# Optimization experiments

Measured on AMD Instinct MI355X. Metric: run time of the kernel, lower is better.

## Reference

```python
import jax, jax.numpy as jnp
import numpy as np

N = 50000   # nodes (single node type)
E = 200000  # edges per relation
R = 2       # relations (etypes)
D = 256     # in_dim == out_dim
H = 8       # heads
DK = D // H # 32
SQRT_DK = float(np.sqrt(DK))


def setup_inputs() -> dict:
    key = jax.random.key(0)
    ks = jax.random.split(key, 12)
    wsc = 1.0 / np.sqrt(D)   # linear-layer scale
    rsc = 1.0 / np.sqrt(DK)  # xavier-ish scale for relation tensors
    return {
        "x": jax.random.normal(ks[0], (N, D), jnp.float32),
        "src": jax.random.randint(ks[1], (R, E), 0, N, jnp.int32),
        "dst": jax.random.randint(ks[2], (R, E), 0, N, jnp.int32),
        "Wk": jax.random.normal(ks[3], (D, D), jnp.float32) * wsc,
        "bk": jnp.zeros((D,), jnp.float32),
        "Wq": jax.random.normal(ks[4], (D, D), jnp.float32) * wsc,
        "bq": jnp.zeros((D,), jnp.float32),
        "Wv": jax.random.normal(ks[5], (D, D), jnp.float32) * wsc,
        "bv": jnp.zeros((D,), jnp.float32),
        "Wa": jax.random.normal(ks[6], (D, D), jnp.float32) * wsc,
        "ba": jnp.zeros((D,), jnp.float32),
        "rel_pri": jnp.ones((R, H), jnp.float32),
        "rel_att": jax.random.normal(ks[7], (R, H, DK, DK), jnp.float32) * rsc,
        "rel_msg": jax.random.normal(ks[8], (R, H, DK, DK), jnp.float32) * rsc,
        "skip": jnp.ones((1,), jnp.float32),
    }


def reference(x, src, dst, Wk, bk, Wq, bq, Wv, bv, Wa, ba, rel_pri, rel_att, rel_msg, skip):
    # Per-type K/Q/V projections (single node type) -> [N,H,DK]
    k = (x @ Wk + bk).reshape(N, H, DK)
    q = (x @ Wq + bq).reshape(N, H, DK)
    v = (x @ Wv + bv).reshape(N, H, DK)

    # edge_attention: per-relation bmm transform of gathered src features
    key_t = jnp.einsum('rehd,rhdf->rehf', k[src], rel_att)   # [R,E,H,DK]
    val = jnp.einsum('rehd,rhdf->rehf', v[src], rel_msg)     # [R,E,H,DK]
    att = (q[dst] * key_t).sum(-1) * rel_pri[:, None, :] / SQRT_DK  # [R,E,H]

    # segment softmax over incoming edges per (relation, dst node)
    seg = (dst + N * jnp.arange(R, dtype=dst.dtype)[:, None]).reshape(-1)  # [R*E]
    att_f = att.reshape(R * E, H)
    m = jax.ops.segment_max(att_f, seg, num_segments=R * N)
    m = jnp.where(jnp.isfinite(m), m, 0.0)  # empty segments -> never gathered
    e = jnp.exp(att_f - m[seg])
    den = jax.ops.segment_sum(e, seg, num_segments=R * N)
    attn = e / den[seg]                                       # [R*E,H]

    # weighted-sum scatter aggregation, then cross_reducer='mean' over relations
    h = jax.ops.segment_sum(attn[:, :, None] * val.reshape(R * E, H, DK), seg,
                            num_segments=R * N)               # [R*N,H,DK]
    t = h.reshape(R, N, D).mean(axis=0)                        # [N,D]

    # skip-gated output projection (dropout inactive in eval, use_norm=False)
    alpha = jax.nn.sigmoid(skip[0])
    return (t @ Wa + ba) * alpha + x * (1.0 - alpha)
```

## Files before the change

kernel.cpp:

```cpp
#include <hip/hip_runtime.h>
#include <hip/hip_bf16.h>
#include <math.h>

#define NN 50000
#define EE 200000
#define DD 256
#define HH 8
#define DKK 32
#define NSEG (2 * NN)
#define SCAN_BLOCKS ((NSEG + 1023) / 1024)
#define MPAD 50048
#define LDQKV 1280

constexpr float RSQRT_DK = 0.17677669529663687f;

__device__ __forceinline__ float bf_lo(unsigned u) { return __uint_as_float(u << 16); }
__device__ __forceinline__ float bf_hi(unsigned u) { return __uint_as_float(u & 0xffff0000u); }
__device__ __forceinline__ unsigned short f2bf(float f) {
    unsigned u = __float_as_uint(f);
    return (unsigned short)((u + 0x7fffu + ((u >> 16) & 1u)) >> 16);
}

typedef __attribute__((ext_vector_type(8))) short bf16x8;
typedef __attribute__((ext_vector_type(4))) float f32x4;

#define GLDS16(g, l)                                                                   \
    __builtin_amdgcn_global_load_lds((const __attribute__((address_space(1))) unsigned int*)(g), \
                                     (__attribute__((address_space(3))) unsigned int*)(l), 16, 0, 0)

__global__ void cast_x_kernel(const float* __restrict__ x, unsigned short* __restrict__ xb) {
    const size_t i = ((size_t)blockIdx.x * 256 + threadIdx.x) * 4;
    float4 v = *(const float4*)&x[i];
    ushort4 o;
    o.x = f2bf(v.x); o.y = f2bf(v.y); o.z = f2bf(v.z); o.w = f2bf(v.w);
    *(ushort4*)&xb[i] = o;
}

__global__ void fold_qkv_kernel(const float* __restrict__ Wq, const float* __restrict__ Wk,
                                const float* __restrict__ Wv, const float* __restrict__ bq,
                                const float* __restrict__ bk, const float* __restrict__ bv,
                                const float* __restrict__ rel_att, const float* __restrict__ rel_msg,
                                unsigned short* __restrict__ Wt, float* __restrict__ bb) {
    const int n = blockIdx.x, kk = threadIdx.x;
    if (n < 256) {
        Wt[(size_t)n * 256 + kk] = f2bf(Wq[(size_t)kk * 256 + n]);
        if (kk == 0) bb[n] = bq[n];
        return;
    }
    const int sec = (n - 256) >> 8;
    const int c = (n - 256) & 255;
    const int h = c >> 5, f = c & 31;
    const float* W    = (sec < 2) ? Wk : Wv;
    const float* bsrc = (sec < 2) ? bk : bv;
    const float* T = ((sec < 2) ? rel_att : rel_msg)
                   + (size_t)(sec & 1) * HH * DKK * DKK + (size_t)h * DKK * DKK + f;
    const float* wrow = &W[(size_t)kk * 256 + h * 32];
    float s = 0.f;
    #pragma unroll
    for (int d = 0; d < 32; ++d) s += wrow[d] * T[(size_t)d * 32];
    Wt[(size_t)n * 256 + kk] = f2bf(s);
    if (kk == 0) {
        float sb = 0.f;
        for (int d = 0; d < 32; ++d) sb += bsrc[h * 32 + d] * T[(size_t)d * 32];
        bb[n] = sb;
    }
}

__global__ void cast_wa_kernel(const float* __restrict__ Wa, unsigned short* __restrict__ Bt) {
    const int n = blockIdx.x, kk = threadIdx.x;
    Bt[(size_t)n * 256 + kk] = f2bf(Wa[(size_t)kk * 256 + n]);
}

__global__ __launch_bounds__(256) void mfma_gemm(
        const unsigned short* __restrict__ A, const unsigned short* __restrict__ Bt,
        const float* __restrict__ bias,
        unsigned short* __restrict__ Cbf, float* __restrict__ Cf,
        int M, int ldc, const float* __restrict__ xres, const float* __restrict__ skip) {
    __shared__ __align__(16) unsigned short As[3][8][64][8];
    __shared__ __align__(16) unsigned short Bs[3][8][64][8];
    const int t = threadIdx.x;
    const int w = t >> 6, l = t & 63;

    const int nwg = gridDim.x * gridDim.y;
    int lin = blockIdx.y * gridDim.x + blockIdx.x;
    {
        const int xcd = lin & 7, pos = lin >> 3;
        const int q = nwg >> 3, r = nwg & 7;
        lin = (xcd < r ? xcd * (q + 1) : r * (q + 1) + (xcd - r) * q) + pos;
    }
    const int n0 = (lin % gridDim.x) * 128;
    const int m0 = (lin / gridDim.x) * 128;
    const int wm = w & 1, wn = w >> 1;

    const int sr = l & 15, sq = l >> 4;
    const unsigned short* ga0 = A  + (size_t)(m0 + w * 16 + sr) * 256 + sq * 8;
    const unsigned short* ga1 = A  + (size_t)(m0 + (w + 4) * 16 + sr) * 256 + sq * 8;
    const unsigned short* gb0 = Bt + (size_t)(n0 + w * 16 + sr) * 256 + sq * 8;
    const unsigned short* gb1 = Bt + (size_t)(n0 + (w + 4) * 16 + sr) * 256 + sq * 8;

#define STAGE(buf, k0) do {                    \
        GLDS16(ga0 + (k0), &As[buf][w][0][0]); \
        GLDS16(ga1 + (k0), &As[buf][w + 4][0][0]); \
        GLDS16(gb0 + (k0), &Bs[buf][w][0][0]); \
        GLDS16(gb1 + (k0), &Bs[buf][w + 4][0][0]); } while (0)

    f32x4 acc[4][4];
    #pragma unroll
    for (int mi = 0; mi < 4; ++mi)
        #pragma unroll
        for (int ni = 0; ni < 4; ++ni) acc[mi][ni] = (f32x4){0.f, 0.f, 0.f, 0.f};

    STAGE(0, 0);
    STAGE(1, 32);
    #pragma unroll
    for (int it = 0; it < 8; ++it) {
        if (it < 7) { asm volatile("s_waitcnt vmcnt(4)" ::: "memory"); }
        else        { asm volatile("s_waitcnt vmcnt(0)" ::: "memory"); }
        __builtin_amdgcn_s_barrier();
        __builtin_amdgcn_sched_barrier(0);
        if (it < 6) {
            STAGE((it + 2) % 3, (it + 2) * 32);
        }
        const int b = it % 3;
        bf16x8 af[4], bfr[4];
        #pragma unroll
        for (int i = 0; i < 4; ++i) {
            af[i]  = *(const bf16x8*)&As[b][wm * 4 + i][l][0];
            bfr[i] = *(const bf16x8*)&Bs[b][wn * 4 + i][l][0];
        }
        #pragma unroll
        for (int mi = 0; mi < 4; ++mi)
            #pragma unroll
            for (int ni = 0; ni < 4; ++ni)
                acc[mi][ni] = __builtin_amdgcn_mfma_f32_16x16x32_bf16(af[mi], bfr[ni],
                                                                      acc[mi][ni], 0, 0, 0);
    }
    __syncthreads();

    unsigned short* ep = (w < 2) ? &As[0][0][0][0] : &Bs[0][0][0][0];
    ep += (w & 1) * 4096;
    const int q4 = l >> 4, c15 = l & 15;

    if (Cf == nullptr) {
        #pragma unroll
        for (int ni = 0; ni < 4; ++ni) {
            const float bcol = bias[n0 + wn * 64 + ni * 16 + c15];
            const int g = ni * 2 + (c15 >> 3);
            #pragma unroll
            for (int mi = 0; mi < 4; ++mi)
                #pragma unroll
                for (int p = 0; p < 4; ++p) {
                    const int row = mi * 16 + q4 * 4 + p;
                    ep[row * 64 + ((g ^ (row & 7)) << 3) + (c15 & 7)] =
                        f2bf(acc[mi][ni][p] + bcol);
                }
        }
        __syncthreads();
        const int rs = l >> 3, cc = l & 7;
        #pragma unroll
        for (int i = 0; i < 8; ++i) {
            const int rl = i * 8 + rs;
            const int row = m0 + wm * 64 + rl;
            if (row < M) {
                uint4 v = *(const uint4*)&ep[rl * 64 + ((cc ^ (rl & 7)) << 3)];
                *(uint4*)&Cbf[(size_t)row * (size_t)ldc + n0 + wn * 64 + cc * 8] = v;
            }
        }
    } else {
        const float alpha = 1.f / (1.f + __expf(-skip[0]));
        const float beta = 1.f - alpha;
        float* epf = (float*)ep;
        #pragma unroll
        for (int half = 0; half < 2; ++half) {
            __syncthreads();
            #pragma unroll
            for (int mi2 = 0; mi2 < 2; ++mi2) {
                const int mi = half * 2 + mi2;
                #pragma unroll
                for (int ni = 0; ni < 4; ++ni) {
                    const float bcol = bias[n0 + wn * 64 + ni * 16 + c15];
                    const int g = ni * 4 + (c15 >> 2);
                    #pragma unroll
                    for (int p = 0; p < 4; ++p) {
                        const int row = mi2 * 16 + q4 * 4 + p;
                        epf[row * 64 + ((g ^ (row & 7)) << 2) + (c15 & 3)] =
                            acc[mi][ni][p] + bcol;
                    }
                }
            }
            __syncthreads();
            const int cc = l & 15, rs = l >> 4;
            #pragma unroll
            for (int i = 0; i < 8; ++i) {
                const int rl = i * 4 + rs;
                const int row = m0 + wm * 64 + half * 32 + rl;
                if (row < M) {
                    const int col = n0 + wn * 64 + cc * 4;
                    float4 v = *(const float4*)&epf[rl * 64 + ((cc ^ (rl & 7)) << 2)];
                    float4 xr = *(const float4*)&xres[(size_t)row * 256 + col];
                    v.x = v.x * alpha + xr.x * beta;
                    v.y = v.y * alpha + xr.y * beta;
                    v.z = v.z * alpha + xr.z * beta;
                    v.w = v.w * alpha + xr.w * beta;
                    *(float4*)&Cf[(size_t)row * 256 + col] = v;
                }
            }
        }
    }
#undef STAGE
}

__global__ void count_kernel(const int* __restrict__ dst, int* __restrict__ cnt) {
    int e = blockIdx.x * 256 + threadIdx.x;
    if (e < 2 * EE) atomicAdd(&cnt[(e / EE) * NN + dst[e]], 1);
}

__global__ __launch_bounds__(1024) void scan_local_kernel(const int* __restrict__ cnt,
                                                          int* __restrict__ rowptr,
                                                          int* __restrict__ bsum) {
    __shared__ int sh[1024];
    const int t = threadIdx.x;
    const int idx = blockIdx.x * 1024 + t;
    const int c = (idx < NSEG) ? cnt[idx] : 0;
    sh[t] = c;
    __syncthreads();
    #pragma unroll
    for (int ofs = 1; ofs < 1024; ofs <<= 1) {
        int v = (t >= ofs) ? sh[t - ofs] : 0;
        __syncthreads();
        sh[t] += v;
        __syncthreads();
    }
    if (idx < NSEG) rowptr[idx] = sh[t] - c;
    if (t == 1023) bsum[blockIdx.x] = sh[1023];
}

__global__ void scan_bsum_kernel(int* __restrict__ bsum, int* __restrict__ rowptr) {
    __shared__ int sh[128];
    const int t = threadIdx.x;
    const int v = (t < SCAN_BLOCKS) ? bsum[t] : 0;
    sh[t] = v;
    __syncthreads();
    #pragma unroll
    for (int ofs = 1; ofs < 128; ofs <<= 1) {
        int u = (t >= ofs) ? sh[t - ofs] : 0;
        __syncthreads();
        sh[t] += u;
        __syncthreads();
    }
    if (t < SCAN_BLOCKS) bsum[t] = sh[t] - v;
    if (t == 127) rowptr[NSEG] = sh[127];
}

__global__ __launch_bounds__(1024) void scan_add_kernel(int* __restrict__ rowptr,
                                                        const int* __restrict__ bsum,
                                                        int* __restrict__ cursor) {
    const int idx = blockIdx.x * 1024 + threadIdx.x;
    if (idx < NSEG) {
        const int v = rowptr[idx] + bsum[blockIdx.x];
        rowptr[idx] = v;
        cursor[idx] = v;
    }
}

__global__ void scatter_kernel(const int* __restrict__ src, const int* __restrict__ dst,
                               int* __restrict__ cursor, int* __restrict__ csr_src) {
    int e = blockIdx.x * 256 + threadIdx.x;
    if (e >= 2 * EE) return;
    int seg = (e / EE) * NN + dst[e];
    int pos = atomicAdd(&cursor[seg], 1);
    csr_src[pos] = src[e];
}

__global__ void node_agg_kernel(const unsigned short* __restrict__ qkv,
                                const int* __restrict__ csr_src,
                                const int* __restrict__ rowptr,
                                const float* __restrict__ pri,
                                unsigned short* __restrict__ tt_bf) {
    const int wave = threadIdx.x >> 6, lane = threadIdx.x & 63;
    const int n = blockIdx.x * 4 + wave;
    const int h = lane >> 3;
    const int off = lane * 4;

    const uint2 qv = *(const uint2*)&qkv[(size_t)n * LDQKV + off];
    const float q0 = bf_lo(qv.x), q1 = bf_hi(qv.x), q2 = bf_lo(qv.y), q3 = bf_hi(qv.y);

    float4 tot = make_float4(0.f, 0.f, 0.f, 0.f);
    #pragma unroll
    for (int r = 0; r < 2; ++r) {
        const float prm = pri[r * HH + h] * RSQRT_DK;
        const int seg = r * NN + n;
        const int j0 = rowptr[seg], j1 = rowptr[seg + 1];
        const size_t kbase = 256 + (size_t)r * 256 + off;
        const size_t vbase = 768 + (size_t)r * 256 + off;
        float4 acc = make_float4(0.f, 0.f, 0.f, 0.f);
        float den = 0.f;
        for (int j = j0; j < j1; ++j) {
            const int s = csr_src[j];
            const size_t rowb = (size_t)s * LDQKV;
            const uint2 kv = *(const uint2*)&qkv[rowb + kbase];
            const uint2 vv = *(const uint2*)&qkv[rowb + vbase];
            float p = q0 * bf_lo(kv.x) + q1 * bf_hi(kv.x)
                    + q2 * bf_lo(kv.y) + q3 * bf_hi(kv.y);
            p += __shfl_xor(p, 1);
            p += __shfl_xor(p, 2);
            p += __shfl_xor(p, 4);
            const float a = __expf(p * prm);
            den += a;
            acc.x += a * bf_lo(vv.x);
            acc.y += a * bf_hi(vv.x);
            acc.z += a * bf_lo(vv.y);
            acc.w += a * bf_hi(vv.y);
        }
        const float wgt = (den > 0.f) ? 0.5f / den : 0.f;
        tot.x += acc.x * wgt; tot.y += acc.y * wgt;
        tot.z += acc.z * wgt; tot.w += acc.w * wgt;
    }
    ushort4 ob;
    ob.x = f2bf(tot.x); ob.y = f2bf(tot.y); ob.z = f2bf(tot.z); ob.w = f2bf(tot.w);
    *(ushort4*)&tt_bf[(size_t)n * 256 + off] = ob;
}

extern "C" void kernel_launch(void* const* d_in, const int* in_sizes, int n_in,
                              void* d_out, int out_size, void* d_ws, size_t ws_size,
                              hipStream_t stream) {
    const float* x       = (const float*)d_in[0];
    const int*   src     = (const int*)d_in[1];
    const int*   dst     = (const int*)d_in[2];
    const float* Wk      = (const float*)d_in[3];
    const float* bk      = (const float*)d_in[4];
    const float* Wq      = (const float*)d_in[5];
    const float* bq      = (const float*)d_in[6];
    const float* Wv      = (const float*)d_in[7];
    const float* bv      = (const float*)d_in[8];
    const float* Wa      = (const float*)d_in[9];
    const float* ba      = (const float*)d_in[10];
    const float* rel_pri = (const float*)d_in[11];
    const float* rel_att = (const float*)d_in[12];
    const float* rel_msg = (const float*)d_in[13];
    const float* skip    = (const float*)d_in[14];
    float* out = (float*)d_out;
    char* ws = (char*)d_ws;

    const size_t ND = (size_t)NN * DD;
    size_t off = 0;
    unsigned short* x_bf   = (unsigned short*)(ws + off); off += (size_t)MPAD * DD * 2;
    unsigned short* qkv_bf = (unsigned short*)(ws + off); off += (size_t)NN * LDQKV * 2;
    unsigned short* tt_bf  = (unsigned short*)(ws + off); off += (size_t)MPAD * DD * 2;
    unsigned short* wqkv_t = (unsigned short*)(ws + off); off += (size_t)LDQKV * 256 * 2;
    unsigned short* wa_t   = (unsigned short*)(ws + off); off += (size_t)256 * 256 * 2;
    float*          bb     = (float*)(ws + off);          off += LDQKV * 4;
    int*            cnt    = (int*)(ws + off);            off += (size_t)NSEG * 4;
    int*            rowptr = (int*)(ws + off);            off += (size_t)(NSEG + 1) * 4;
    int*            cursor = (int*)(ws + off);            off += (size_t)NSEG * 4;
    int*            bsum   = (int*)(ws + off);            off += 128 * 4;
    int*            csr_src= (int*)(ws + off);            off += (size_t)2 * EE * 4;
    if (ws_size < off) return;

    cast_x_kernel<<<(int)(ND / 1024), 256, 0, stream>>>(x, x_bf);
    fold_qkv_kernel<<<LDQKV, 256, 0, stream>>>(Wq, Wk, Wv, bq, bk, bv,
                                               rel_att, rel_msg, wqkv_t, bb);
    cast_wa_kernel<<<256, 256, 0, stream>>>(Wa, wa_t);

    dim3 g_qkv(LDQKV / 128, MPAD / 128);
    mfma_gemm<<<g_qkv, 256, 0, stream>>>(x_bf, wqkv_t, bb, qkv_bf, nullptr,
                                         NN, LDQKV, nullptr, nullptr);

    hipMemsetAsync(cnt, 0, (size_t)NSEG * 4, stream);
    const int eg = (2 * EE + 255) / 256;
    count_kernel<<<eg, 256, 0, stream>>>(dst, cnt);
    scan_local_kernel<<<SCAN_BLOCKS, 1024, 0, stream>>>(cnt, rowptr, bsum);
    scan_bsum_kernel<<<1, 128, 0, stream>>>(bsum, rowptr);
    scan_add_kernel<<<SCAN_BLOCKS, 1024, 0, stream>>>(rowptr, bsum, cursor);
    scatter_kernel<<<eg, 256, 0, stream>>>(src, dst, cursor, csr_src);

    node_agg_kernel<<<NN / 4, 256, 0, stream>>>(qkv_bf, csr_src, rowptr,
                                                rel_pri, tt_bf);

    dim3 g_out(DD / 128, MPAD / 128);
    mfma_gemm<<<g_out, 256, 0, stream>>>(tt_bf, wa_t, ba, nullptr, out,
                                         NN, DD, x, skip);
}
```

Measured before the change: 377.2 us.

## Split node aggregation across relations and edge halves with prefetch; fuse Wa cast

The node aggregation kernel now gives each relation its own wave, and each wave splits into two half-waves that take alternating edges. Each lane loads 16 bytes of K and V and prefetches the next edge's rows. The two relation partial sums are combined through shared memory after a block barrier. The separate Wa transpose-cast kernel is folded into the fold_qkv launch as extra blocks, removing one launch. This is meant to raise memory-level parallelism and occupancy on the irregular gathers, at the cost of an LDS round-trip, a sync, and half the lanes sitting idle during the final write.

```diff
diff --git a/kernel.cpp b/kernel.cpp
--- a/kernel.cpp
+++ b/kernel.cpp
@@ -40,8 +40,14 @@
                                 const float* __restrict__ Wv, const float* __restrict__ bq,
                                 const float* __restrict__ bk, const float* __restrict__ bv,
                                 const float* __restrict__ rel_att, const float* __restrict__ rel_msg,
+                                const float* __restrict__ Wa, unsigned short* __restrict__ wa_t,
                                 unsigned short* __restrict__ Wt, float* __restrict__ bb) {
     const int n = blockIdx.x, kk = threadIdx.x;
+    if (n >= 1280) {
+        const int nn = n - 1280;
+        wa_t[(size_t)nn * 256 + kk] = f2bf(Wa[(size_t)kk * 256 + nn]);
+        return;
+    }
     if (n < 256) {
         Wt[(size_t)n * 256 + kk] = f2bf(Wq[(size_t)kk * 256 + n]);
         if (kk == 0) bb[n] = bq[n];
@@ -64,11 +70,6 @@
         for (int d = 0; d < 32; ++d) sb += bsrc[h * 32 + d] * T[(size_t)d * 32];
         bb[n] = sb;
     }
-}
-
-__global__ void cast_wa_kernel(const float* __restrict__ Wa, unsigned short* __restrict__ Bt) {
-    const int n = blockIdx.x, kk = threadIdx.x;
-    Bt[(size_t)n * 256 + kk] = f2bf(Wa[(size_t)kk * 256 + n]);
 }
 
 __global__ __launch_bounds__(256) void mfma_gemm(
@@ -272,53 +273,93 @@
     csr_src[pos] = src[e];
 }
 
-__global__ void node_agg_kernel(const unsigned short* __restrict__ qkv,
-                                const int* __restrict__ csr_src,
-                                const int* __restrict__ rowptr,
-                                const float* __restrict__ pri,
-                                unsigned short* __restrict__ tt_bf) {
-    const int wave = threadIdx.x >> 6, lane = threadIdx.x & 63;
-    const int n = blockIdx.x * 4 + wave;
-    const int h = lane >> 3;
-    const int off = lane * 4;
-
-    const uint2 qv = *(const uint2*)&qkv[(size_t)n * LDQKV + off];
+__global__ __launch_bounds__(512) void node_agg_kernel(
+        const unsigned short* __restrict__ qkv,
+        const int* __restrict__ csr_src,
+        const int* __restrict__ rowptr,
+        const float* __restrict__ pri,
+        unsigned short* __restrict__ tt_bf) {
+    __shared__ float sh[4][256];
+    const int w = threadIdx.x >> 6, lane = threadIdx.x & 63;
+    const int nl = w >> 1, r = w & 1;
+    const int n = blockIdx.x * 4 + nl;
+    const int lh = lane & 31;
+    const int eh = lane >> 5;
+    const int h = lh >> 2;
+    const size_t coff = (size_t)lh * 8;
+
+    const uint4 qv = *(const uint4*)&qkv[(size_t)n * LDQKV + coff];
     const float q0 = bf_lo(qv.x), q1 = bf_hi(qv.x), q2 = bf_lo(qv.y), q3 = bf_hi(qv.y);
-
-    float4 tot = make_float4(0.f, 0.f, 0.f, 0.f);
-    #pragma unroll
-    for (int r = 0; r < 2; ++r) {
-        const float prm = pri[r * HH + h] * RSQRT_DK;
-        const int seg = r * NN + n;
-        const int j0 = rowptr[seg], j1 = rowptr[seg + 1];
-        const size_t kbase = 256 + (size_t)r * 256 + off;
-        const size_t vbase = 768 + (size_t)r * 256 + off;
-        float4 acc = make_float4(0.f, 0.f, 0.f, 0.f);
-        float den = 0.f;
-        for (int j = j0; j < j1; ++j) {
-            const int s = csr_src[j];
-            const size_t rowb = (size_t)s * LDQKV;
-            const uint2 kv = *(const uint2*)&qkv[rowb + kbase];
-            const uint2 vv = *(const uint2*)&qkv[rowb + vbase];
-            float p = q0 * bf_lo(kv.x) + q1 * bf_hi(kv.x)
-                    + q2 * bf_lo(kv.y) + q3 * bf_hi(kv.y);
-            p += __shfl_xor(p, 1);
-            p += __shfl_xor(p, 2);
-            p += __shfl_xor(p, 4);
-            const float a = __expf(p * prm);
-            den += a;
-            acc.x += a * bf_lo(vv.x);
-            acc.y += a * bf_hi(vv.x);
-            acc.z += a * bf_lo(vv.y);
-            acc.w += a * bf_hi(vv.y);
-        }
-        const float wgt = (den > 0.f) ? 0.5f / den : 0.f;
-        tot.x += acc.x * wgt; tot.y += acc.y * wgt;
-        tot.z += acc.z * wgt; tot.w += acc.w * wgt;
-    }
-    ushort4 ob;
-    ob.x = f2bf(tot.x); ob.y = f2bf(tot.y); ob.z = f2bf(tot.z); ob.w = f2bf(tot.w);
-    *(ushort4*)&tt_bf[(size_t)n * 256 + off] = ob;
+    const float q4_ = bf_lo(qv.z), q5 = bf_hi(qv.z), q6 = bf_lo(qv.w), q7 = bf_hi(qv.w);
+
+    const float prm = pri[r * HH + h] * RSQRT_DK;
+    const int seg = r * NN + n;
+    const int j0 = rowptr[seg], j1 = rowptr[seg + 1];
+    const size_t kbase = 256 + (size_t)r * 256 + coff;
+    const size_t vbase = 768 + (size_t)r * 256 + coff;
+
+    float a0 = 0.f, a1 = 0.f, a2 = 0.f, a3 = 0.f, a4 = 0.f, a5 = 0.f, a6 = 0.f, a7 = 0.f;
+    float den = 0.f;
+
+    int j = j0 + eh;
+    uint4 kv, vv;
+    bool valid = j < j1;
+    if (valid) {
+        const size_t rowb = (size_t)csr_src[j] * LDQKV;
+        kv = *(const uint4*)&qkv[rowb + kbase];
+        vv = *(const uint4*)&qkv[rowb + vbase];
+    }
+    while (valid) {
+        const int jn = j + 2;
+        const bool validn = jn < j1;
+        uint4 kvn, vvn;
+        if (validn) {
+            const size_t rowb = (size_t)csr_src[jn] * LDQKV;
+            kvn = *(const uint4*)&qkv[rowb + kbase];
+            vvn = *(const uint4*)&qkv[rowb + vbase];
+        }
+        float p = q0 * bf_lo(kv.x) + q1 * bf_hi(kv.x) + q2 * bf_lo(kv.y) + q3 * bf_hi(kv.y)
+                + q4_ * bf_lo(kv.z) + q5 * bf_hi(kv.z) + q6 * bf_lo(kv.w) + q7 * bf_hi(kv.w);
+        p += __shfl_xor(p, 1);
+        p += __shfl_xor(p, 2);
+        const float a = __expf(p * prm);
+        den += a;
+        a0 += a * bf_lo(vv.x); a1 += a * bf_hi(vv.x);
+        a2 += a * bf_lo(vv.y); a3 += a * bf_hi(vv.y);
+        a4 += a * bf_lo(vv.z); a5 += a * bf_hi(vv.z);
+        a6 += a * bf_lo(vv.w); a7 += a * bf_hi(vv.w);
+        kv = kvn; vv = vvn; j = jn; valid = validn;
+    }
+    den += __shfl_xor(den, 32);
+    a0 += __shfl_xor(a0, 32); a1 += __shfl_xor(a1, 32);
+    a2 += __shfl_xor(a2, 32); a3 += __shfl_xor(a3, 32);
+    a4 += __shfl_xor(a4, 32); a5 += __shfl_xor(a5, 32);
+    a6 += __shfl_xor(a6, 32); a7 += __shfl_xor(a7, 32);
+    const float wgt = (den > 0.f) ? 0.5f / den : 0.f;
+
+    if (r == 0 && eh == 0) {
+        sh[nl][0 * 32 + lh] = a0 * wgt; sh[nl][1 * 32 + lh] = a1 * wgt;
+        sh[nl][2 * 32 + lh] = a2 * wgt; sh[nl][3 * 32 + lh] = a3 * wgt;
+        sh[nl][4 * 32 + lh] = a4 * wgt; sh[nl][5 * 32 + lh] = a5 * wgt;
+        sh[nl][6 * 32 + lh] = a6 * wgt; sh[nl][7 * 32 + lh] = a7 * wgt;
+    }
+    __syncthreads();
+    if (r == 1 && eh == 0) {
+        const float t0 = sh[nl][0 * 32 + lh] + a0 * wgt;
+        const float t1 = sh[nl][1 * 32 + lh] + a1 * wgt;
+        const float t2 = sh[nl][2 * 32 + lh] + a2 * wgt;
+        const float t3 = sh[nl][3 * 32 + lh] + a3 * wgt;
+        const float t4 = sh[nl][4 * 32 + lh] + a4 * wgt;
+        const float t5 = sh[nl][5 * 32 + lh] + a5 * wgt;
+        const float t6 = sh[nl][6 * 32 + lh] + a6 * wgt;
+        const float t7 = sh[nl][7 * 32 + lh] + a7 * wgt;
+        uint4 o;
+        o.x = (unsigned)f2bf(t0) | ((unsigned)f2bf(t1) << 16);
+        o.y = (unsigned)f2bf(t2) | ((unsigned)f2bf(t3) << 16);
+        o.z = (unsigned)f2bf(t4) | ((unsigned)f2bf(t5) << 16);
+        o.w = (unsigned)f2bf(t6) | ((unsigned)f2bf(t7) << 16);
+        *(uint4*)&tt_bf[(size_t)n * 256 + coff] = o;
+    }
 }
 
 extern "C" void kernel_launch(void* const* d_in, const int* in_sizes, int n_in,
@@ -358,9 +399,8 @@
     if (ws_size < off) return;
 
     cast_x_kernel<<<(int)(ND / 1024), 256, 0, stream>>>(x, x_bf);
-    fold_qkv_kernel<<<LDQKV, 256, 0, stream>>>(Wq, Wk, Wv, bq, bk, bv,
-                                               rel_att, rel_msg, wqkv_t, bb);
-    cast_wa_kernel<<<256, 256, 0, stream>>>(Wa, wa_t);
+    fold_qkv_kernel<<<1536, 256, 0, stream>>>(Wq, Wk, Wv, bq, bk, bv,
+                                              rel_att, rel_msg, Wa, wa_t, wqkv_t, bb);
 
     dim3 g_qkv(LDQKV / 128, MPAD / 128);
     mfma_gemm<<<g_qkv, 256, 0, stream>>>(x_bf, wqkv_t, bb, qkv_bf, nullptr,
@@ -374,7 +414,7 @@
     scan_add_kernel<<<SCAN_BLOCKS, 1024, 0, stream>>>(rowptr, bsum, cursor);
     scatter_kernel<<<eg, 256, 0, stream>>>(src, dst, cursor, csr_src);
 
-    node_agg_kernel<<<NN / 4, 256, 0, stream>>>(qkv_bf, csr_src, rowptr,
+    node_agg_kernel<<<NN / 4, 512, 0, stream>>>(qkv_bf, csr_src, rowptr,
                                                 rel_pri, tt_bf);
 
     dim3 g_out(DD / 128, MPAD / 128);
```

After: 374.2 us. No clear change (-0.8%).
